# Kernel tuning notes

Hardware: AMD Instinct MI355X
Metric: run time of the kernel (lower is better)

Reference implementation:

```python
import jax, jax.numpy as jnp
import numpy as np

N = 100000      # nodes
E = 1600000     # edges (avg degree 16)
D_IN = 128
CONV_SIZES = [64, 64]
FC_SIZES = [64, 32, 1]


def _glorot(key, shape):
    lim = np.sqrt(6.0 / (shape[0] + shape[1]))
    return jax.random.uniform(key, shape, jnp.float32, -lim, lim)


def setup_inputs() -> dict:
    key = jax.random.key(0)
    ks = jax.random.split(key, 2 + len(CONV_SIZES) + len(FC_SIZES))
    inp = {
        "x": jax.random.normal(ks[0], (N, D_IN), jnp.float32),
        "edge_index": jax.random.randint(ks[1], (2, E), 0, N, dtype=jnp.int64),
    }
    size = D_IN
    ki = 2
    for li, s in enumerate(CONV_SIZES):
        inp[f"cW{li}"] = _glorot(ks[ki], (size, s)); ki += 1
        inp[f"cb{li}"] = jnp.zeros((s,), jnp.float32)
        size = s
    for li, s in enumerate(FC_SIZES):
        inp[f"fW{li}"] = _glorot(ks[ki], (size, s)); ki += 1
        inp[f"fb{li}"] = jnp.zeros((s,), jnp.float32)
        size = s
    return inp


def gcn_conv(x, src, dst, W, b, n_nodes):
    """PyG GCNConv: symmetric normalization with added self-loops."""
    xl = x @ W  # [N, out]
    # degree including self-loop
    deg = jnp.zeros((n_nodes,), xl.dtype).at[dst].add(1.0) + 1.0
    dinv = jax.lax.rsqrt(deg)
    norm = dinv[src] * dinv[dst]                 # [E]
    msg = xl[src] * norm[:, None]                # gather + scale, [E, out]
    agg = jax.ops.segment_sum(msg, dst, num_segments=n_nodes)
    # self-loop contribution: norm = 1/deg
    return agg + xl * (1.0 / deg)[:, None] + b


def reference(x, edge_index, cW0, cb0, cW1, cb1, fW0, fb0, fW1, fb1, fW2, fb2):
    src, dst = edge_index[0], edge_index[1]
    h = jnp.tanh(gcn_conv(x, src, dst, cW0, cb0, N))
    h = jnp.tanh(gcn_conv(h, src, dst, cW1, cb1, N))
    h = jnp.tanh(h @ fW0 + fb0)
    h = jnp.tanh(h @ fW1 + fb1)
    return h @ fW2 + fb2  # [N, 1]
```

## Files before the change

kernel.cpp:

```cpp
#include <hip/hip_runtime.h>
#include <math.h>

#define N_NODES 100000
#define N_EDGES 1600000
#define NB     391
#define CHUNK  4096
#define NBLK_A 391

typedef unsigned short ushort_t;
typedef __attribute__((ext_vector_type(2))) float f2v;

__device__ inline unsigned short f2bf(float f) {
    unsigned u = __float_as_uint(f);
    unsigned r = (u + 0x7FFFu + ((u >> 16) & 1u)) >> 16;
    return (unsigned short)r;
}
__device__ inline void accp(f2v& a, unsigned u) {
    f2v t;
    t.x = __uint_as_float(u << 16);
    t.y = __uint_as_float(u & 0xFFFF0000u);
    a += t;
}
__device__ inline float fast_tanh(float x) {
    float e = __expf(2.0f * x);
    return fmaf(-2.0f, __builtin_amdgcn_rcpf(e + 1.0f), 1.0f);
}


__global__ __launch_bounds__(256) void k_count(const int* __restrict__ dst,
                                               unsigned* __restrict__ cnt) {
    __shared__ unsigned h[NB];
    const int tid = threadIdx.x;
    const long e0 = (long)blockIdx.x * CHUNK;
    for (int i = tid; i < NB; i += 256) h[i] = 0u;
    __syncthreads();
    for (int i = tid; i < CHUNK; i += 256) {
        long e = e0 + i;
        if (e < N_EDGES) atomicAdd(&h[((unsigned)dst[e]) >> 8], 1u);
    }
    __syncthreads();
    for (int b = tid; b < NB; b += 256) cnt[b * NBLK_A + blockIdx.x] = h[b];
}

__global__ __launch_bounds__(512) void k_bucket_scan(unsigned* __restrict__ cnt,
                                                     unsigned* __restrict__ btot) {
    __shared__ unsigned s[512];
    const int tid = threadIdx.x;
    const int b = blockIdx.x;
    unsigned v = (tid < NBLK_A) ? cnt[b * NBLK_A + tid] : 0u;
    s[tid] = v;
    __syncthreads();
    for (int o = 1; o < 512; o <<= 1) {
        unsigned t = (tid >= o) ? s[tid - o] : 0u;
        __syncthreads();
        s[tid] += t;
        __syncthreads();
    }
    if (tid < NBLK_A) cnt[b * NBLK_A + tid] = s[tid] - v;
    if (tid == NBLK_A - 1) btot[b] = s[tid];
}

__global__ __launch_bounds__(512) void k_scan_bkt(const unsigned* __restrict__ btot,
                                                  unsigned* __restrict__ bktbase) {
    __shared__ unsigned s[512];
    const int tid = threadIdx.x;
    unsigned v = (tid < NB) ? btot[tid] : 0u;
    s[tid] = v;
    __syncthreads();
    for (int o = 1; o < 512; o <<= 1) {
        unsigned t = (tid >= o) ? s[tid - o] : 0u;
        __syncthreads();
        s[tid] += t;
        __syncthreads();
    }
    if (tid < NB) bktbase[tid] = s[tid] - v;
    if (tid == NB - 1) bktbase[NB] = s[tid];
}

__global__ __launch_bounds__(256) void k_bin(const int* __restrict__ src,
                                             const int* __restrict__ dst,
                                             const unsigned* __restrict__ cnt,
                                             const unsigned* __restrict__ bktbase,
                                             unsigned* __restrict__ binned) {
    __shared__ unsigned cntA[NB];
    __shared__ unsigned excl[NB];
    __shared__ unsigned gbase[NB];
    __shared__ unsigned scanbuf[512];
    __shared__ unsigned data[CHUNK];
    const int tid = threadIdx.x;
    const long e0 = (long)blockIdx.x * CHUNK;

    for (int i = tid; i < NB; i += 256) cntA[i] = 0u;
    __syncthreads();
    for (int i = tid; i < CHUNK; i += 256) {
        long e = e0 + i;
        if (e < N_EDGES) atomicAdd(&cntA[((unsigned)dst[e]) >> 8], 1u);
    }
    __syncthreads();
    scanbuf[tid] = (tid < NB) ? cntA[tid] : 0u;
    scanbuf[tid + 256] = (tid + 256 < NB) ? cntA[tid + 256] : 0u;
    __syncthreads();
    for (int o = 1; o < 512; o <<= 1) {
        unsigned v0 = (tid >= o) ? scanbuf[tid - o] : 0u;
        unsigned v1 = (tid + 256 >= o) ? scanbuf[tid + 256 - o] : 0u;
        __syncthreads();
        scanbuf[tid] += v0;
        scanbuf[tid + 256] += v1;
        __syncthreads();
    }
    for (int b = tid; b < NB; b += 256) {
        excl[b] = scanbuf[b] - cntA[b];
        gbase[b] = bktbase[b] + cnt[b * NBLK_A + blockIdx.x];
    }
    __syncthreads();
    for (int i = tid; i < NB; i += 256) cntA[i] = 0u;
    __syncthreads();
    for (int i = tid; i < CHUNK; i += 256) {
        long e = e0 + i;
        if (e < N_EDGES) {
            unsigned d = (unsigned)dst[e];
            unsigned b = d >> 8;
            unsigned slot = excl[b] + atomicAdd(&cntA[b], 1u);
            data[slot] = (((unsigned)src[e]) << 8) | (d & 255u);
        }
    }
    __syncthreads();
    const int w = tid >> 6, lane = tid & 63;
    for (int b = w; b < NB; b += 4) {
        unsigned c = cntA[b];
        unsigned sb = excl[b], gb = gbase[b];
        for (unsigned k = lane; k < c; k += 64)
            binned[gb + k] = data[sb + k];
    }
}

__global__ __launch_bounds__(256) void k_csr_fill2(const unsigned* __restrict__ binned,
                                                   const unsigned* __restrict__ bktbase,
                                                   unsigned* __restrict__ rowptr,
                                                   float* __restrict__ dinv,
                                                   int* __restrict__ ssrc) {
    __shared__ unsigned cnt[256];
    __shared__ unsigned s[256];
    __shared__ unsigned cur[256];
    const int b = blockIdx.x;
    const int tid = threadIdx.x;
    const int n0 = b * 256;
    const unsigned beg = bktbase[b], end = bktbase[b + 1];
    cnt[tid] = 0u;
    __syncthreads();
    for (unsigned i = beg + tid; i < end; i += 256)
        atomicAdd(&cnt[binned[i] & 255u], 1u);
    __syncthreads();
    const unsigned v = cnt[tid];
    s[tid] = v;
    __syncthreads();
    for (int o = 1; o < 256; o <<= 1) {
        unsigned t = (tid >= o) ? s[tid - o] : 0u;
        __syncthreads();
        s[tid] += t;
        __syncthreads();
    }
    const unsigned excl = s[tid] - v;
    const int node = n0 + tid;
    if (node < N_NODES) {
        rowptr[node] = beg + excl;
        dinv[node] = rsqrtf((float)(v + 1u));
        if (node == N_NODES - 1) rowptr[N_NODES] = end;
    }
    cur[tid] = beg + excl;
    __syncthreads();
    for (unsigned i = beg + tid; i < end; i += 256) {
        unsigned p = binned[i];
        unsigned pos = atomicAdd(&cur[p & 255u], 1u);
        ssrc[pos] = (int)(p >> 8);
    }
}


template<int K, int OUT>
__global__ __launch_bounds__(256) void k_gemm_bf(const float* __restrict__ A,
                                                 const float* __restrict__ W,
                                                 const float* __restrict__ dinv,
                                                 ushort_t* __restrict__ C) {
    constexpr int BR = 32;
    __shared__ float Wld[K * OUT];
    __shared__ float Ald[BR * K];
    const int tid = threadIdx.x;
    for (int i = tid; i < K * OUT; i += 256) Wld[i] = W[i];
    const long row0 = (long)blockIdx.x * BR;
    const float4* A4 = reinterpret_cast<const float4*>(A + row0 * K);
    float4* Ald4w = reinterpret_cast<float4*>(Ald);
    constexpr int NV = BR * K / 4;
    for (int i = tid; i < NV; i += 256) Ald4w[i] = A4[i];
    __syncthreads();

    constexpr int RG = 256 / OUT;
    constexpr int RPT = BR / RG;
    const int col = tid % OUT;
    const int rg = tid / OUT;
    const float4* Ald4 = reinterpret_cast<const float4*>(Ald);
    float acc[RPT];
#pragma unroll
    for (int j = 0; j < RPT; ++j) acc[j] = 0.f;
    for (int k4 = 0; k4 < K; k4 += 4) {
        const float w0 = Wld[(k4 + 0) * OUT + col];
        const float w1 = Wld[(k4 + 1) * OUT + col];
        const float w2 = Wld[(k4 + 2) * OUT + col];
        const float w3 = Wld[(k4 + 3) * OUT + col];
#pragma unroll
        for (int j = 0; j < RPT; ++j) {
            const float4 a = Ald4[((rg + j * RG) * K + k4) >> 2];
            acc[j] = fmaf(a.x, w0, fmaf(a.y, w1, fmaf(a.z, w2, fmaf(a.w, w3, acc[j]))));
        }
    }
#pragma unroll
    for (int j = 0; j < RPT; ++j) {
        const long r = row0 + rg + j * RG;
        C[r * OUT + col] = f2bf(acc[j] * dinv[r]);
    }
}

__global__ __launch_bounds__(256) void k_agg(const ushort_t* __restrict__ xlb,
                                             const float* __restrict__ dinv,
                                             const unsigned* __restrict__ rowptr,
                                             const int* __restrict__ ssrc,
                                             const float* __restrict__ bias,
                                             float* __restrict__ h) {
    const int node = blockIdx.x * 4 + (threadIdx.x >> 6);
    const int lane = threadIdx.x & 63;
    const int g = lane >> 4;
    const int l = lane & 15;
    const uint2* xb2 = reinterpret_cast<const uint2*>(xlb);

    const unsigned beg = rowptr[node], end = rowptr[node + 1];
    f2v a0 = {0.f, 0.f}, a1 = {0.f, 0.f};
    f2v b0 = {0.f, 0.f}, b1 = {0.f, 0.f};
    if (g == 0) {
        const uint2 v = xb2[(size_t)node * 16 + l];
        accp(a0, v.x); accp(a1, v.y);
    }
    unsigned j = beg + g;
    for (; j + 4 < end; j += 8) {
        const int s0i = ssrc[j];
        const int s1i = ssrc[j + 4];
        const uint2 v0 = xb2[(size_t)s0i * 16 + l];
        const uint2 v1 = xb2[(size_t)s1i * 16 + l];
        accp(a0, v0.x); accp(a1, v0.y);
        accp(b0, v1.x); accp(b1, v1.y);
    }
    if (j < end) {
        const uint2 v = xb2[(size_t)ssrc[j] * 16 + l];
        accp(a0, v.x); accp(a1, v.y);
    }
    a0 += b0; a1 += b1;
    float s0 = a0.x, s1 = a0.y, s2 = a1.x, s3 = a1.y;
    s0 += __shfl_xor(s0, 16); s1 += __shfl_xor(s1, 16);
    s2 += __shfl_xor(s2, 16); s3 += __shfl_xor(s3, 16);
    s0 += __shfl_xor(s0, 32); s1 += __shfl_xor(s1, 32);
    s2 += __shfl_xor(s2, 32); s3 += __shfl_xor(s3, 32);
    const float t01 = (g & 1) ? s1 : s0;
    const float t23 = (g & 1) ? s3 : s2;
    const float v = (g & 2) ? t23 : t01;
    const int f = l * 4 + g;
    const float r = fast_tanh(fmaf(v, dinv[node], bias[f]));
    h[(size_t)node * 64 + f] = r;
}

__global__ __launch_bounds__(256, 4) void k_fc(const float* __restrict__ h2,
                                               const float* __restrict__ fW0, const float* __restrict__ fb0,
                                               const float* __restrict__ fW1, const float* __restrict__ fb1,
                                               const float* __restrict__ fW2, const float* __restrict__ fb2,
                                               float* __restrict__ out) {
    constexpr int BR = 32;
    constexpr int LDH = 68;
    __shared__ float W0[64 * 64];
    __shared__ float W1[64 * 32];
    __shared__ float Hin[BR * LDH];
    __shared__ float Ht[BR * LDH];
    __shared__ float Hs[BR * 33];
    __shared__ float W2s[33];
    const int tid = threadIdx.x;
    {
        const float4* w04 = reinterpret_cast<const float4*>(fW0);
        float4* W04 = reinterpret_cast<float4*>(W0);
        for (int i = tid; i < 64 * 16; i += 256) W04[i] = w04[i];
        const float4* w14 = reinterpret_cast<const float4*>(fW1);
        float4* W14 = reinterpret_cast<float4*>(W1);
        for (int i = tid; i < 64 * 8; i += 256) W14[i] = w14[i];
        if (tid < 32) W2s[tid] = fW2[tid];
        if (tid == 32) W2s[32] = fb2[0];
    }
    const long row0 = (long)blockIdx.x * BR;
    {
        const float4* H4 = reinterpret_cast<const float4*>(h2 + row0 * 64);
        for (int i = tid; i < BR * 16; i += 256) {
            int r = i >> 4, q = i & 15;
            *reinterpret_cast<float4*>(&Hin[r * LDH + q * 4]) = H4[i];
        }
    }
    __syncthreads();

    {
        const int rp = tid >> 4;
        const int cq = tid & 15;
        const int r0 = rp * 2, r1 = r0 + 1;
        const float4 bias = reinterpret_cast<const float4*>(fb0)[cq];
        float4 acc0 = bias, acc1 = bias;
#pragma unroll 2
        for (int k4 = 0; k4 < 64; k4 += 4) {
            const float4 a0 = *reinterpret_cast<const float4*>(&Hin[r0 * LDH + k4]);
            const float4 a1 = *reinterpret_cast<const float4*>(&Hin[r1 * LDH + k4]);
            const float4 w0 = *reinterpret_cast<const float4*>(&W0[(k4 + 0) * 64 + cq * 4]);
            const float4 w1 = *reinterpret_cast<const float4*>(&W0[(k4 + 1) * 64 + cq * 4]);
            const float4 w2 = *reinterpret_cast<const float4*>(&W0[(k4 + 2) * 64 + cq * 4]);
            const float4 w3 = *reinterpret_cast<const float4*>(&W0[(k4 + 3) * 64 + cq * 4]);
            acc0.x = fmaf(a0.x, w0.x, fmaf(a0.y, w1.x, fmaf(a0.z, w2.x, fmaf(a0.w, w3.x, acc0.x))));
            acc0.y = fmaf(a0.x, w0.y, fmaf(a0.y, w1.y, fmaf(a0.z, w2.y, fmaf(a0.w, w3.y, acc0.y))));
            acc0.z = fmaf(a0.x, w0.z, fmaf(a0.y, w1.z, fmaf(a0.z, w2.z, fmaf(a0.w, w3.z, acc0.z))));
            acc0.w = fmaf(a0.x, w0.w, fmaf(a0.y, w1.w, fmaf(a0.z, w2.w, fmaf(a0.w, w3.w, acc0.w))));
            acc1.x = fmaf(a1.x, w0.x, fmaf(a1.y, w1.x, fmaf(a1.z, w2.x, fmaf(a1.w, w3.x, acc1.x))));
            acc1.y = fmaf(a1.x, w0.y, fmaf(a1.y, w1.y, fmaf(a1.z, w2.y, fmaf(a1.w, w3.y, acc1.y))));
            acc1.z = fmaf(a1.x, w0.z, fmaf(a1.y, w1.z, fmaf(a1.z, w2.z, fmaf(a1.w, w3.z, acc1.z))));
            acc1.w = fmaf(a1.x, w0.w, fmaf(a1.y, w1.w, fmaf(a1.z, w2.w, fmaf(a1.w, w3.w, acc1.w))));
        }
        float4 t0, t1;
        t0.x = fast_tanh(acc0.x); t0.y = fast_tanh(acc0.y);
        t0.z = fast_tanh(acc0.z); t0.w = fast_tanh(acc0.w);
        t1.x = fast_tanh(acc1.x); t1.y = fast_tanh(acc1.y);
        t1.z = fast_tanh(acc1.z); t1.w = fast_tanh(acc1.w);
        *reinterpret_cast<float4*>(&Ht[r0 * LDH + cq * 4]) = t0;
        *reinterpret_cast<float4*>(&Ht[r1 * LDH + cq * 4]) = t1;
    }
    __syncthreads();

    {
        const int r = tid >> 3;
        const int cq = tid & 7;
        const float4 bias = reinterpret_cast<const float4*>(fb1)[cq];
        float4 acc0 = bias;
#pragma unroll 2
        for (int k4 = 0; k4 < 64; k4 += 4) {
            const float4 a0 = *reinterpret_cast<const float4*>(&Ht[r * LDH + k4]);
            const float4 w0 = *reinterpret_cast<const float4*>(&W1[(k4 + 0) * 32 + cq * 4]);
            const float4 w1 = *reinterpret_cast<const float4*>(&W1[(k4 + 1) * 32 + cq * 4]);
            const float4 w2 = *reinterpret_cast<const float4*>(&W1[(k4 + 2) * 32 + cq * 4]);
            const float4 w3 = *reinterpret_cast<const float4*>(&W1[(k4 + 3) * 32 + cq * 4]);
            acc0.x = fmaf(a0.x, w0.x, fmaf(a0.y, w1.x, fmaf(a0.z, w2.x, fmaf(a0.w, w3.x, acc0.x))));
            acc0.y = fmaf(a0.x, w0.y, fmaf(a0.y, w1.y, fmaf(a0.z, w2.y, fmaf(a0.w, w3.y, acc0.y))));
            acc0.z = fmaf(a0.x, w0.z, fmaf(a0.y, w1.z, fmaf(a0.z, w2.z, fmaf(a0.w, w3.z, acc0.z))));
            acc0.w = fmaf(a0.x, w0.w, fmaf(a0.y, w1.w, fmaf(a0.z, w2.w, fmaf(a0.w, w3.w, acc0.w))));
        }
        Hs[r * 33 + cq * 4 + 0] = fast_tanh(acc0.x);
        Hs[r * 33 + cq * 4 + 1] = fast_tanh(acc0.y);
        Hs[r * 33 + cq * 4 + 2] = fast_tanh(acc0.z);
        Hs[r * 33 + cq * 4 + 3] = fast_tanh(acc0.w);
    }
    __syncthreads();

    if (tid < BR) {
        float a = W2s[32];
        for (int k = 0; k < 32; ++k) a = fmaf(Hs[tid * 33 + k], W2s[k], a);
        out[row0 + tid] = a;
    }
}


extern "C" void kernel_launch(void* const* d_in, const int* in_sizes, int n_in,
                              void* d_out, int out_size, void* d_ws, size_t ws_size,
                              hipStream_t stream) {
    const float* x    = (const float*)d_in[0];
    const int*   eidx = (const int*)d_in[1];
    const float* cW0  = (const float*)d_in[2];
    const float* cb0  = (const float*)d_in[3];
    const float* cW1  = (const float*)d_in[4];
    const float* cb1  = (const float*)d_in[5];
    const float* fW0  = (const float*)d_in[6];
    const float* fb0  = (const float*)d_in[7];
    const float* fW1  = (const float*)d_in[8];
    const float* fb1  = (const float*)d_in[9];
    const float* fW2  = (const float*)d_in[10];
    const float* fb2  = (const float*)d_in[11];
    float* out = (float*)d_out;

    const int* src = eidx;
    const int* dst = eidx + N_EDGES;

    char* ws = (char*)d_ws;
    unsigned* rowptr  = (unsigned*)(ws);
    float*    dinv    = (float*)   (ws + 400016);
    unsigned* cnt     = (unsigned*)(ws + 800016);
    unsigned* btot    = (unsigned*)(ws + 1411552);
    unsigned* bktbase = (unsigned*)(ws + 1413120);
    int*      ssrc    = (int*)     (ws + 1414688);
    ushort_t* xlb     = (ushort_t*)(ws + 7814688);
    unsigned* binned  = (unsigned*)(ws + 20614688);
    float*    bufB    = (float*)   (ws + 27014688);

    const int gRow = N_NODES / 32;
    const int gAgg = N_NODES / 4;

    k_count<<<NBLK_A, 256, 0, stream>>>(dst, cnt);
    k_bucket_scan<<<NB, 512, 0, stream>>>(cnt, btot);
    k_scan_bkt<<<1, 512, 0, stream>>>(btot, bktbase);
    k_bin<<<NBLK_A, 256, 0, stream>>>(src, dst, cnt, bktbase, binned);
    k_csr_fill2<<<NB, 256, 0, stream>>>(binned, bktbase, rowptr, dinv, ssrc);

    k_gemm_bf<128, 64><<<gRow, 256, 0, stream>>>(x, cW0, dinv, xlb);
    k_agg<<<gAgg, 256, 0, stream>>>(xlb, dinv, rowptr, ssrc, cb0, bufB);
    k_gemm_bf<64, 64><<<gRow, 256, 0, stream>>>(bufB, cW1, dinv, xlb);
    k_agg<<<gAgg, 256, 0, stream>>>(xlb, dinv, rowptr, ssrc, cb1, bufB);
    k_fc<<<gRow, 256, 0, stream>>>(bufB, fW0, fb0, fW1, fb1, fW2, fb2, out);
}
```

Measured before the change: 270.3 us.

## Register-tile the dense GEMM 4x4 per thread and unroll aggregation gathers deeper

The node-feature GEMM now uses 64-row blocks, with each thread computing a 4x4 output tile from float4 shared-memory loads. The A tile is padded (K+4) to avoid LDS bank conflicts, and each thread stores four bf16 outputs with one packed write, which cuts LDS traffic per FMA. The aggregation loop now issues four neighbour gathers per iteration instead of two, giving more memory-level parallelism, with a loop remainder for the tail. A shared fma4 helper tidies the FC kernel. The larger tile uses more LDS (about 49KB for K=128), which may reduce occupancy.

```diff
diff --git a/kernel.cpp b/kernel.cpp
--- a/kernel.cpp
+++ b/kernel.cpp
@@ -24,6 +24,14 @@
 __device__ inline float fast_tanh(float x) {
     float e = __expf(2.0f * x);
     return fmaf(-2.0f, __builtin_amdgcn_rcpf(e + 1.0f), 1.0f);
+}
+__device__ inline void fma4(float4& acc, const float4 a,
+                            const float4 w0, const float4 w1,
+                            const float4 w2, const float4 w3) {
+    acc.x = fmaf(a.x, w0.x, fmaf(a.y, w1.x, fmaf(a.z, w2.x, fmaf(a.w, w3.x, acc.x))));
+    acc.y = fmaf(a.x, w0.y, fmaf(a.y, w1.y, fmaf(a.z, w2.y, fmaf(a.w, w3.y, acc.y))));
+    acc.z = fmaf(a.x, w0.z, fmaf(a.y, w1.z, fmaf(a.z, w2.z, fmaf(a.w, w3.z, acc.z))));
+    acc.w = fmaf(a.x, w0.w, fmaf(a.y, w1.w, fmaf(a.z, w2.w, fmaf(a.w, w3.w, acc.w))));
 }
 
 
@@ -177,46 +185,65 @@
 }
 
 
-template<int K, int OUT>
+template<int K>
 __global__ __launch_bounds__(256) void k_gemm_bf(const float* __restrict__ A,
                                                  const float* __restrict__ W,
                                                  const float* __restrict__ dinv,
                                                  ushort_t* __restrict__ C) {
-    constexpr int BR = 32;
+    constexpr int OUT = 64;
+    constexpr int BR = 64;
+    constexpr int LDA = K + 4;
     __shared__ float Wld[K * OUT];
-    __shared__ float Ald[BR * K];
-    const int tid = threadIdx.x;
-    for (int i = tid; i < K * OUT; i += 256) Wld[i] = W[i];
-    const long row0 = (long)blockIdx.x * BR;
-    const float4* A4 = reinterpret_cast<const float4*>(A + row0 * K);
-    float4* Ald4w = reinterpret_cast<float4*>(Ald);
-    constexpr int NV = BR * K / 4;
-    for (int i = tid; i < NV; i += 256) Ald4w[i] = A4[i];
-    __syncthreads();
-
-    constexpr int RG = 256 / OUT;
-    constexpr int RPT = BR / RG;
-    const int col = tid % OUT;
-    const int rg = tid / OUT;
-    const float4* Ald4 = reinterpret_cast<const float4*>(Ald);
-    float acc[RPT];
+    __shared__ float Ald[BR * LDA];
+    const int tid = threadIdx.x;
+    const int row0 = blockIdx.x * BR;
+    const int nrows = (N_NODES - row0 < BR) ? (N_NODES - row0) : BR;
+
+    {
+        const float4* W4 = reinterpret_cast<const float4*>(W);
+        float4* Wl4 = reinterpret_cast<float4*>(Wld);
+        for (int i = tid; i < K * OUT / 4; i += 256) Wl4[i] = W4[i];
+        const float4* A4 = reinterpret_cast<const float4*>(A + (size_t)row0 * K);
+        const int nv = nrows * (K / 4);
+        for (int i = tid; i < nv; i += 256) {
+            int r = i / (K / 4), q = i % (K / 4);
+            *reinterpret_cast<float4*>(&Ald[r * LDA + q * 4]) = A4[i];
+        }
+    }
+    __syncthreads();
+
+    const int tr = tid >> 4;
+    const int tc = tid & 15;
+    const int r0 = tr * 4;
+    float4 acc0 = {0,0,0,0}, acc1 = {0,0,0,0}, acc2 = {0,0,0,0}, acc3 = {0,0,0,0};
+#pragma unroll 2
+    for (int k4 = 0; k4 < K; k4 += 4) {
+        const float4 a0 = *reinterpret_cast<const float4*>(&Ald[(r0 + 0) * LDA + k4]);
+        const float4 a1 = *reinterpret_cast<const float4*>(&Ald[(r0 + 1) * LDA + k4]);
+        const float4 a2 = *reinterpret_cast<const float4*>(&Ald[(r0 + 2) * LDA + k4]);
+        const float4 a3 = *reinterpret_cast<const float4*>(&Ald[(r0 + 3) * LDA + k4]);
+        const float4 w0 = *reinterpret_cast<const float4*>(&Wld[(k4 + 0) * OUT + tc * 4]);
+        const float4 w1 = *reinterpret_cast<const float4*>(&Wld[(k4 + 1) * OUT + tc * 4]);
+        const float4 w2 = *reinterpret_cast<const float4*>(&Wld[(k4 + 2) * OUT + tc * 4]);
+        const float4 w3 = *reinterpret_cast<const float4*>(&Wld[(k4 + 3) * OUT + tc * 4]);
+        fma4(acc0, a0, w0, w1, w2, w3);
+        fma4(acc1, a1, w0, w1, w2, w3);
+        fma4(acc2, a2, w0, w1, w2, w3);
+        fma4(acc3, a3, w0, w1, w2, w3);
+    }
+    float4 accs[4] = {acc0, acc1, acc2, acc3};
 #pragma unroll
-    for (int j = 0; j < RPT; ++j) acc[j] = 0.f;
-    for (int k4 = 0; k4 < K; k4 += 4) {
-        const float w0 = Wld[(k4 + 0) * OUT + col];
-        const float w1 = Wld[(k4 + 1) * OUT + col];
-        const float w2 = Wld[(k4 + 2) * OUT + col];
-        const float w3 = Wld[(k4 + 3) * OUT + col];
-#pragma unroll
-        for (int j = 0; j < RPT; ++j) {
-            const float4 a = Ald4[((rg + j * RG) * K + k4) >> 2];
-            acc[j] = fmaf(a.x, w0, fmaf(a.y, w1, fmaf(a.z, w2, fmaf(a.w, w3, acc[j]))));
-        }
-    }
-#pragma unroll
-    for (int j = 0; j < RPT; ++j) {
-        const long r = row0 + rg + j * RG;
-        C[r * OUT + col] = f2bf(acc[j] * dinv[r]);
+    for (int i = 0; i < 4; ++i) {
+        const int r = r0 + i;
+        if (r < nrows) {
+            const float di = dinv[row0 + r];
+            ushort4 o;
+            o.x = f2bf(accs[i].x * di);
+            o.y = f2bf(accs[i].y * di);
+            o.z = f2bf(accs[i].z * di);
+            o.w = f2bf(accs[i].w * di);
+            *reinterpret_cast<ushort4*>(&C[(size_t)(row0 + r) * OUT + tc * 4]) = o;
+        }
     }
 }
 
@@ -240,15 +267,21 @@
         accp(a0, v.x); accp(a1, v.y);
     }
     unsigned j = beg + g;
-    for (; j + 4 < end; j += 8) {
+    for (; j + 12 < end; j += 16) {
         const int s0i = ssrc[j];
         const int s1i = ssrc[j + 4];
+        const int s2i = ssrc[j + 8];
+        const int s3i = ssrc[j + 12];
         const uint2 v0 = xb2[(size_t)s0i * 16 + l];
         const uint2 v1 = xb2[(size_t)s1i * 16 + l];
+        const uint2 v2 = xb2[(size_t)s2i * 16 + l];
+        const uint2 v3 = xb2[(size_t)s3i * 16 + l];
         accp(a0, v0.x); accp(a1, v0.y);
         accp(b0, v1.x); accp(b1, v1.y);
-    }
-    if (j < end) {
+        accp(a0, v2.x); accp(a1, v2.y);
+        accp(b0, v3.x); accp(b1, v3.y);
+    }
+    for (; j < end; j += 4) {
         const uint2 v = xb2[(size_t)ssrc[j] * 16 + l];
         accp(a0, v.x); accp(a1, v.y);
     }
@@ -314,14 +347,8 @@
             const float4 w1 = *reinterpret_cast<const float4*>(&W0[(k4 + 1) * 64 + cq * 4]);
             const float4 w2 = *reinterpret_cast<const float4*>(&W0[(k4 + 2) * 64 + cq * 4]);
             const float4 w3 = *reinterpret_cast<const float4*>(&W0[(k4 + 3) * 64 + cq * 4]);
-            acc0.x = fmaf(a0.x, w0.x, fmaf(a0.y, w1.x, fmaf(a0.z, w2.x, fmaf(a0.w, w3.x, acc0.x))));
-            acc0.y = fmaf(a0.x, w0.y, fmaf(a0.y, w1.y, fmaf(a0.z, w2.y, fmaf(a0.w, w3.y, acc0.y))));
-            acc0.z = fmaf(a0.x, w0.z, fmaf(a0.y, w1.z, fmaf(a0.z, w2.z, fmaf(a0.w, w3.z, acc0.z))));
-            acc0.w = fmaf(a0.x, w0.w, fmaf(a0.y, w1.w, fmaf(a0.z, w2.w, fmaf(a0.w, w3.w, acc0.w))));
-            acc1.x = fmaf(a1.x, w0.x, fmaf(a1.y, w1.x, fmaf(a1.z, w2.x, fmaf(a1.w, w3.x, acc1.x))));
-            acc1.y = fmaf(a1.x, w0.y, fmaf(a1.y, w1.y, fmaf(a1.z, w2.y, fmaf(a1.w, w3.y, acc1.y))));
-            acc1.z = fmaf(a1.x, w0.z, fmaf(a1.y, w1.z, fmaf(a1.z, w2.z, fmaf(a1.w, w3.z, acc1.z))));
-            acc1.w = fmaf(a1.x, w0.w, fmaf(a1.y, w1.w, fmaf(a1.z, w2.w, fmaf(a1.w, w3.w, acc1.w))));
+            fma4(acc0, a0, w0, w1, w2, w3);
+            fma4(acc1, a1, w0, w1, w2, w3);
         }
         float4 t0, t1;
         t0.x = fast_tanh(acc0.x); t0.y = fast_tanh(acc0.y);
@@ -345,10 +372,7 @@
             const float4 w1 = *reinterpret_cast<const float4*>(&W1[(k4 + 1) * 32 + cq * 4]);
             const float4 w2 = *reinterpret_cast<const float4*>(&W1[(k4 + 2) * 32 + cq * 4]);
             const float4 w3 = *reinterpret_cast<const float4*>(&W1[(k4 + 3) * 32 + cq * 4]);
-            acc0.x = fmaf(a0.x, w0.x, fmaf(a0.y, w1.x, fmaf(a0.z, w2.x, fmaf(a0.w, w3.x, acc0.x))));
-            acc0.y = fmaf(a0.x, w0.y, fmaf(a0.y, w1.y, fmaf(a0.z, w2.y, fmaf(a0.w, w3.y, acc0.y))));
-            acc0.z = fmaf(a0.x, w0.z, fmaf(a0.y, w1.z, fmaf(a0.z, w2.z, fmaf(a0.w, w3.z, acc0.z))));
-            acc0.w = fmaf(a0.x, w0.w, fmaf(a0.y, w1.w, fmaf(a0.z, w2.w, fmaf(a0.w, w3.w, acc0.w))));
+            fma4(acc0, a0, w0, w1, w2, w3);
         }
         Hs[r * 33 + cq * 4 + 0] = fast_tanh(acc0.x);
         Hs[r * 33 + cq * 4 + 1] = fast_tanh(acc0.y);
@@ -397,6 +421,7 @@
     float*    bufB    = (float*)   (ws + 27014688);
 
     const int gRow = N_NODES / 32;
+    const int gGemm = (N_NODES + 63) / 64;
     const int gAgg = N_NODES / 4;
 
     k_count<<<NBLK_A, 256, 0, stream>>>(dst, cnt);
@@ -405,9 +430,9 @@
     k_bin<<<NBLK_A, 256, 0, stream>>>(src, dst, cnt, bktbase, binned);
     k_csr_fill2<<<NB, 256, 0, stream>>>(binned, bktbase, rowptr, dinv, ssrc);
 
-    k_gemm_bf<128, 64><<<gRow, 256, 0, stream>>>(x, cW0, dinv, xlb);
+    k_gemm_bf<128><<<gGemm, 256, 0, stream>>>(x, cW0, dinv, xlb);
     k_agg<<<gAgg, 256, 0, stream>>>(xlb, dinv, rowptr, ssrc, cb0, bufB);
-    k_gemm_bf<64, 64><<<gRow, 256, 0, stream>>>(bufB, cW1, dinv, xlb);
+    k_gemm_bf<64><<<gGemm, 256, 0, stream>>>(bufB, cW1, dinv, xlb);
     k_agg<<<gAgg, 256, 0, stream>>>(xlb, dinv, rowptr, ssrc, cb1, bufB);
     k_fc<<<gRow, 256, 0, stream>>>(bufB, fW0, fb0, fW1, fb1, fW2, fb2, out);
 }
```

New measurement: 256.2 us. -5.2%, faster.
